# Kernel optimization log

Hardware: AMD Instinct MI355X
Metric: run time of the kernel (lower is better)

Reference implementation:

```python
import jax, jax.numpy as jnp
import numpy as np

DIM = 256
HEADS = 8
HEAD_DIM = DIM // HEADS
B = 4
Wd, Hd = 48, 48
N = Wd * Hd  # 2304


def _layernorm(x, g, b, eps=1e-5):
    mu = jnp.mean(x, axis=-1, keepdims=True)
    var = jnp.mean(jnp.square(x - mu), axis=-1, keepdims=True)
    return (x - mu) * jax.lax.rsqrt(var + eps) * g + b


def _build_mask(mask):
    # Binarize: <1 -> 0, >0 -> 1 (identity on {0,1} inputs)
    m = (mask > 0).astype(jnp.float32)
    flat = m.reshape(B, m.shape[1], Hd * Wd)[:, 0, :]  # [B, N]
    # mask[b,i,j] zeroed where (flat[j]==0 & flat[i]==1) | (flat[j]==0 & flat[i]==0)
    col0 = flat[:, None, :] == 0   # varies along j
    row = flat[:, :, None]         # varies along i
    bad = (col0 & (row == 1)) | (col0 & (row == 0))
    return (~bad).astype(jnp.float32)  # [B, N, N]


def setup_inputs() -> dict:
    key = jax.random.key(0)
    ks = jax.random.split(key, 12)
    s = 0.02
    x = jax.random.normal(ks[0], (B, N, DIM), jnp.float32)
    mask = jax.random.randint(ks[1], (B, 1, Wd, Hd), 0, 2).astype(jnp.float32)
    inp = {
        "x": x,
        "mask": mask,
        "ln_g": jnp.ones((DIM,), jnp.float32),
        "ln_b": jnp.zeros((DIM,), jnp.float32),
        "Wq": jax.random.normal(ks[2], (DIM, DIM), jnp.float32) * s,
        "bq": jnp.zeros((DIM,), jnp.float32),
        "Wk": jax.random.normal(ks[3], (DIM, DIM), jnp.float32) * s,
        "bk": jnp.zeros((DIM,), jnp.float32),
        "Wv": jax.random.normal(ks[4], (DIM, DIM), jnp.float32) * s,
        "bv": jnp.zeros((DIM,), jnp.float32),
        "Wp": jax.random.normal(ks[5], (DIM, DIM), jnp.float32) * s,
        "bp": jnp.zeros((DIM,), jnp.float32),
    }
    return inp


def reference(x, mask, ln_g, ln_b, Wq, bq, Wk, bk, Wv, bv, Wp, bp):
    Bx, Nx, C = x.shape
    mask_f = _build_mask(mask)  # [B, N, N]
    xn = _layernorm(x, ln_g, ln_b)
    def heads(Wm, bm):
        return (xn @ Wm + bm).reshape(Bx, Nx, HEADS, HEAD_DIM).transpose(0, 2, 1, 3)
    q = heads(Wq, bq)
    k = heads(Wk, bk)
    v = heads(Wv, bv)
    # NOTE: no 1/sqrt(d) scaling in the original; multiplicative 0/1 mask pre-softmax
    attn = jnp.einsum("bhnd,bhmd->bhnm", q, k) * mask_f[:, None, :, :]
    attn = jax.nn.softmax(attn, axis=-1)
    out = jnp.einsum("bhnm,bhmd->bhnd", attn, v)
    out = out.transpose(0, 2, 1, 3).reshape(Bx, Nx, C)
    return out @ Wp + bp
```

## Files before the change

kernel.cpp:

```cpp
#include <hip/hip_runtime.h>
#include <math.h>

typedef __attribute__((ext_vector_type(8))) short short8;
typedef __attribute__((ext_vector_type(4))) float f32x4;

#if __has_builtin(__builtin_amdgcn_exp2f)
#define EXP2F(x) __builtin_amdgcn_exp2f(x)
#else
#define EXP2F(x) exp2f(x)
#endif

constexpr int B   = 4;
constexpr int N   = 2304;
constexpr int DIM = 256;
constexpr int NH  = 8;
constexpr int DH  = 32;
constexpr int M   = B * N;
constexpr int SLOTS = 2336;
constexpr int CST = SLOTS * DH;
constexpr int XPB = SLOTS * DIM;
constexpr float LOG2E = 1.44269504088896f;

__device__ inline unsigned short f2bf(float f) {
    union { float f; unsigned u; } c; c.f = f;
    unsigned u = c.u;
    u += 0x7fffu + ((u >> 16) & 1u);
    return (unsigned short)(u >> 16);
}
__device__ inline float bf2f(unsigned short h) {
    union { unsigned u; float f; } c; c.u = ((unsigned)h) << 16;
    return c.f;
}
__device__ inline unsigned bits(float f) {
    union { float f; unsigned u; } c; c.f = f; return c.u;
}

__device__ inline size_t fo256(int r, int k) {
    return ((size_t)((r >> 4) * 8 + (k >> 5)) << 9)
         + (size_t)(((((k & 31) >> 3) << 4) + (r & 15)) * 8 + (k & 7));
}
__device__ inline size_t foQK(int n, int d) {
    return ((size_t)(n >> 4) << 9)
         + (size_t)((((d >> 3) << 4) + (n & 15)) * 8 + (d & 7));
}
__device__ inline size_t foKI(int slot, int d) {
    int tile = ((slot >> 5) << 1) + (slot & 1);
    int npos = (slot & 31) >> 1;
    return ((size_t)tile << 9)
         + (size_t)((((d >> 3) << 4) + npos) * 8 + (d & 7));
}
__device__ inline size_t foVTC(int d, int key) {
    return ((size_t)((d >> 4) * (SLOTS / 32) + (key >> 5)) << 9)
         + (size_t)(((((key & 31) >> 3) << 4) + (d & 15)) * 8 + (key & 7));
}

__global__ __launch_bounds__(256) void scan_kernel(
    const float* __restrict__ mask, int* __restrict__ ncp,
    int* __restrict__ fwd, float* __restrict__ vm,
    unsigned short* __restrict__ xph)
{
    __shared__ int wcnt[9][4];
    __shared__ unsigned long long wbal[9][4];
    int b = blockIdx.x;
    int t = threadIdx.x;
    int wave = t >> 6, lane = t & 63;
    vm[b * 256 + t] = 0.f;
    #pragma unroll
    for (int c = 0; c < 9; ++c) {
        int j = c * 256 + t;
        bool keep = mask[(size_t)b * N + j] > 0.f;
        unsigned long long bal = __ballot(keep);
        if (lane == 0) { wcnt[c][wave] = __popcll(bal); wbal[c][wave] = bal; }
    }
    __syncthreads();
    int Nc = 0;
    #pragma unroll
    for (int c = 0; c < 9; ++c)
        Nc += wcnt[c][0] + wcnt[c][1] + wcnt[c][2] + wcnt[c][3];
    int Nkp = (Nc + 31) & ~31;
    int mend = Nkp + (N - Nc);
    if (t == 0) { ncp[b * 2] = Nc; ncp[b * 2 + 1] = Nkp; }
    int base = 0;
    #pragma unroll
    for (int c = 0; c < 9; ++c) {
        int wb = base;
        for (int w = 0; w < wave; ++w) wb += wcnt[c][w];
        unsigned long long bal = wbal[c][wave];
        bool keep = (bal >> lane) & 1ull;
        int pos = __popcll(bal & ((1ull << lane) - 1ull));
        int keptBefore = wb + pos;
        int j = c * 256 + t;
        fwd[(size_t)b * N + j] = keep ? keptBefore : Nkp + (j - keptBefore);
        base += wcnt[c][0] + wcnt[c][1] + wcnt[c][2] + wcnt[c][3];
    }
    int c1 = Nkp - Nc;
    unsigned short* xb = xph + (size_t)b * XPB;
    for (int u = t; u < 32 * 64; u += 256) {
        int pi = u >> 6;
        int kk = (u & 63) * 4;
        int slot = (pi < c1) ? (Nc + pi) : (mend + (pi - c1));
        ushort4 z4 = {0, 0, 0, 0};
        *(ushort4*)&xb[fo256(slot, kk)] = z4;
    }
}

__global__ __launch_bounds__(256) void prep2(
    const float* __restrict__ x, const float* __restrict__ g,
    const float* __restrict__ bta, const int* __restrict__ fwd,
    const float* __restrict__ Wq, const float* __restrict__ Wk,
    const float* __restrict__ Wv, const float* __restrict__ Wp,
    unsigned short* __restrict__ Wth, unsigned short* __restrict__ Wtl,
    unsigned short* __restrict__ xh, unsigned short* __restrict__ xph)
{
    __shared__ float tbuf[32][33];
    int bx = blockIdx.x;
    int t = threadIdx.x;
    if (bx < 256) {
        int z = bx >> 6, w = bx & 63;
        const float* W = (z == 0) ? Wq : (z == 1) ? Wk : (z == 2) ? Wv : Wp;
        unsigned short* oh = Wth + (size_t)z * DIM * DIM;
        unsigned short* ol = Wtl + (size_t)z * DIM * DIM;
        int tx = t & 31, ty0 = t >> 5;
        int n0 = (w & 7) * 32, k0 = (w >> 3) * 32;
        for (int ty = ty0; ty < 32; ty += 8)
            tbuf[ty][tx] = W[(size_t)(k0 + ty) * DIM + n0 + tx];
        __syncthreads();
        for (int nn = ty0; nn < 32; nn += 8) {
            float v = tbuf[tx][nn];
            unsigned short hh = f2bf(v);
            size_t o = fo256(n0 + nn, k0 + tx);
            oh[o] = hh;
            ol[o] = f2bf(v - bf2f(hh));
        }
    } else {
        int wave = t >> 6, lane = t & 63;
        int row = (bx - 256) * 4 + wave;
        float4 v = *(const float4*)&x[(size_t)row * DIM + lane * 4];
        float s = v.x + v.y + v.z + v.w;
        #pragma unroll
        for (int o = 32; o > 0; o >>= 1) s += __shfl_xor(s, o, 64);
        float mu = s * (1.0f / DIM);
        float d0 = v.x - mu, d1 = v.y - mu, d2 = v.z - mu, d3 = v.w - mu;
        float s2 = d0 * d0 + d1 * d1 + d2 * d2 + d3 * d3;
        #pragma unroll
        for (int o = 32; o > 0; o >>= 1) s2 += __shfl_xor(s2, o, 64);
        float r = rsqrtf(s2 * (1.0f / DIM) + 1e-5f);
        float4 gg = *(const float4*)&g[lane * 4];
        float4 bb = *(const float4*)&bta[lane * 4];
        ushort4 hi;
        hi.x = f2bf(d0 * r * gg.x + bb.x);
        hi.y = f2bf(d1 * r * gg.y + bb.y);
        hi.z = f2bf(d2 * r * gg.z + bb.z);
        hi.w = f2bf(d3 * r * gg.w + bb.w);
        *(ushort4*)&xh[fo256(row, lane * 4)] = hi;
        int b = row / N;
        int slot = fwd[row];
        *(ushort4*)&xph[(size_t)b * XPB + fo256(slot, lane * 4)] = hi;
    }
}

__global__ __launch_bounds__(256, 8) void gemm_qkv(
    const unsigned short* __restrict__ xh,
    const unsigned short* __restrict__ xph,
    const unsigned short* __restrict__ Wth,
    const float* __restrict__ bq, const float* __restrict__ bk,
    const float* __restrict__ bv, const int* __restrict__ ncp,
    unsigned short* __restrict__ qb, unsigned short* __restrict__ kc,
    unsigned short* __restrict__ vc, float* __restrict__ vm)
{
    constexpr size_t WSZ = (size_t)DIM * DIM;
    int z = blockIdx.z, bx = blockIdx.x;
    int tid = threadIdx.x;
    int wave = tid >> 6, lane = tid & 63;
    int quad = lane >> 4, l16 = lane & 15;
    const unsigned short *PA, *PB;
    int arow0, brow0, b;
    if (z == 0) {
        if (bx >= 576) return;
        arow0 = (bx >> 3) * 128 + wave * 32;
        brow0 = (bx & 7) * 32;
        b = ((bx >> 3) * 128) / N;
        PA = xh; PB = Wth;
    } else if (z == 1) {
        b = bx / 152;
        int rr = bx % 152;
        arow0 = (rr >> 3) * 128 + wave * 32;
        brow0 = (rr & 7) * 32;
        if (arow0 >= SLOTS) return;
        if (arow0 >= ncp[b * 2 + 1]) return;
        PA = xph + (size_t)b * XPB;
        PB = Wth + WSZ;
    } else {
        if (bx >= 584) return;
        int nidx = bx % 292;
        b = nidx / 73;
        arow0 = (bx / 292) * 128 + wave * 32;
        brow0 = (nidx % 73) * 32;
        PA = Wth + 2 * WSZ;
        PB = xph + (size_t)b * XPB;
    }
    f32x4 acc[2][2] = {};
    #pragma unroll
    for (int k0 = 0; k0 < DIM; k0 += 32) {
        size_t at = (((size_t)(arow0 >> 4) * 8 + (k0 >> 5)) << 9) + lane * 8;
        size_t bt = (((size_t)(brow0 >> 4) * 8 + (k0 >> 5)) << 9) + lane * 8;
        short8 a0 = *(const short8*)&PA[at];
        short8 a1 = *(const short8*)&PA[at + 4096];
        short8 b0 = *(const short8*)&PB[bt];
        short8 b1 = *(const short8*)&PB[bt + 4096];
        acc[0][0] = __builtin_amdgcn_mfma_f32_16x16x32_bf16(a0, b0, acc[0][0], 0, 0, 0);
        acc[0][1] = __builtin_amdgcn_mfma_f32_16x16x32_bf16(a0, b1, acc[0][1], 0, 0, 0);
        acc[1][0] = __builtin_amdgcn_mfma_f32_16x16x32_bf16(a1, b0, acc[1][0], 0, 0, 0);
        acc[1][1] = __builtin_amdgcn_mfma_f32_16x16x32_bf16(a1, b1, acc[1][1], 0, 0, 0);
    }
    if (z == 0) {
        int nbase = arow0 - b * N;
        #pragma unroll
        for (int j = 0; j < 2; ++j) {
            int c = brow0 + j * 16 + l16;
            int h = c >> 5, d = c & 31;
            float bs = bq[c];
            unsigned short* ob = qb + (size_t)(b * NH + h) * ((size_t)N * DH);
            #pragma unroll
            for (int i = 0; i < 2; ++i)
            #pragma unroll
            for (int r = 0; r < 4; ++r) {
                int n = nbase + i * 16 + quad * 4 + r;
                ob[foQK(n, d)] = f2bf((acc[i][j][r] + bs) * LOG2E);
            }
        }
    } else if (z == 1) {
        #pragma unroll
        for (int j = 0; j < 2; ++j) {
            int c = brow0 + j * 16 + l16;
            int h = c >> 5, d = c & 31;
            float bs = bk[c];
            unsigned short* ob = kc + (size_t)(b * NH + h) * CST;
            #pragma unroll
            for (int i = 0; i < 2; ++i)
            #pragma unroll
            for (int r = 0; r < 4; ++r) {
                int slot = arow0 + i * 16 + quad * 4 + r;
                ob[foKI(slot, d)] = f2bf(acc[i][j][r] + bs);
            }
        }
    } else {
        int Nc  = ncp[b * 2];
        int Nkp = ncp[b * 2 + 1];
        int mend = Nkp + (N - Nc);
        bool anymask = (brow0 + 32 > Nkp) && (brow0 < mend);
        #pragma unroll
        for (int i = 0; i < 2; ++i)
        #pragma unroll
        for (int r = 0; r < 4; ++r) {
            int m = arow0 + i * 16 + quad * 4 + r;
            int h = m >> 5, d = m & 31;
            float bs = bv[m];
            unsigned short* ob = vc + (size_t)(b * NH + h) * CST;
            float vsum = 0.f;
            #pragma unroll
            for (int j = 0; j < 2; ++j) {
                int key = brow0 + j * 16 + l16;
                float val = acc[i][j][r] + bs;
                if (key < Nkp) ob[foVTC(d, key)] = f2bf(val);
                else if (key < mend) vsum += val;
            }
            if (anymask) {
                vsum += __shfl_xor(vsum, 1, 64);
                vsum += __shfl_xor(vsum, 2, 64);
                vsum += __shfl_xor(vsum, 4, 64);
                vsum += __shfl_xor(vsum, 8, 64);
                if (l16 == 0) atomicAdd(&vm[(size_t)(b * NH + h) * 32 + d], vsum);
            }
        }
    }
}

__global__ __launch_bounds__(128, 4) void attn_kernel(
    const unsigned short* __restrict__ Qb,
    const unsigned short* __restrict__ Kc,
    const unsigned short* __restrict__ Vc,
    const int* __restrict__ ncp,
    const float* __restrict__ vm,
    unsigned short* __restrict__ ah)
{
    __shared__ unsigned short pbuf[2 * 2 * 640];
    __shared__ float cbuf[64 * 24];
    int tid  = threadIdx.x;
    int kh   = tid >> 6, lane = tid & 63;
    int quad = lane >> 4, l16 = lane & 15;
    int bh = blockIdx.y, b = bh >> 3, h = bh & 7;

    int q0 = blockIdx.x * 32;
    const unsigned short* Qf = Qb + (size_t)bh * ((size_t)N * DH);
    const unsigned short* Kf = Kc + (size_t)bh * CST;
    const unsigned short* Vf = Vc + (size_t)bh * CST;

    int Nc  = ncp[b * 2];
    int Nkp = ncp[b * 2 + 1];
    int chunks = Nkp >> 5;
    int kbeg = ((chunks * kh) >> 1) << 5;
    int kend = ((chunks * (kh + 1)) >> 1) << 5;

    short8 qA0 = *(const short8*)&Qf[((size_t)(q0 >> 4) << 9) + lane * 8];
    short8 qA1 = *(const short8*)&Qf[((size_t)((q0 >> 4) + 1) << 9) + lane * 8];

    f32x4 o00 = {0,0,0,0}, o01 = {0,0,0,0}, o10 = {0,0,0,0}, o11 = {0,0,0,0};
    float l0[4] = {0,0,0,0}, l1[4] = {0,0,0,0};

    unsigned short* pb0 = &pbuf[(kh * 2 + 0) * 640];
    unsigned short* pb1 = &pbuf[(kh * 2 + 1) * 640];

    short8 kB0 = *(const short8*)&Kf[((size_t)(kbeg >> 4) << 9) + lane * 8];
    short8 kB1 = *(const short8*)&Kf[((size_t)((kbeg >> 4) + 1) << 9) + lane * 8];
    short8 vB0 = *(const short8*)&Vf[((size_t)(kbeg >> 5) << 9) + lane * 8];
    short8 vB1 = *(const short8*)&Vf[((size_t)((SLOTS / 32) + (kbeg >> 5)) << 9) + lane * 8];

    for (int k0 = kbeg; k0 < kend; k0 += 32) {
        int kn = (k0 + 32 < kend) ? k0 + 32 : kbeg;
        short8 nk0 = *(const short8*)&Kf[((size_t)(kn >> 4) << 9) + lane * 8];
        short8 nk1 = *(const short8*)&Kf[((size_t)((kn >> 4) + 1) << 9) + lane * 8];
        short8 nv0 = *(const short8*)&Vf[((size_t)(kn >> 5) << 9) + lane * 8];
        short8 nv1 = *(const short8*)&Vf[((size_t)((SLOTS / 32) + (kn >> 5)) << 9) + lane * 8];

        int key0 = k0 + 2 * l16;
        bool in0 = key0 < Nc;
        bool in1 = key0 + 1 < Nc;
        f32x4 z = {0,0,0,0};
        f32x4 s00 = __builtin_amdgcn_mfma_f32_16x16x32_bf16(qA0, kB0, z, 0, 0, 0);
        f32x4 s01 = __builtin_amdgcn_mfma_f32_16x16x32_bf16(qA0, kB1, z, 0, 0, 0);
        f32x4 s10 = __builtin_amdgcn_mfma_f32_16x16x32_bf16(qA1, kB0, z, 0, 0, 0);
        f32x4 s11 = __builtin_amdgcn_mfma_f32_16x16x32_bf16(qA1, kB1, z, 0, 0, 0);
        #pragma unroll
        for (int r = 0; r < 4; ++r) {
            int row = quad * 4 + r;
            float p00 = in0 ? EXP2F(s00[r]) : 0.f;
            float p01 = in1 ? EXP2F(s01[r]) : 0.f;
            float p10 = in0 ? EXP2F(s10[r]) : 0.f;
            float p11 = in1 ? EXP2F(s11[r]) : 0.f;
            l0[r] += p00 + p01;
            l1[r] += p10 + p11;
            unsigned pk0 = (bits(p00) >> 16) | (bits(p01) & 0xffff0000u);
            unsigned pk1 = (bits(p10) >> 16) | (bits(p11) & 0xffff0000u);
            *(unsigned*)&pb0[row * 40 + 2 * l16] = pk0;
            *(unsigned*)&pb1[row * 40 + 2 * l16] = pk1;
        }
        short8 pA0 = *(const short8*)&pb0[l16 * 40 + quad * 8];
        short8 pA1 = *(const short8*)&pb1[l16 * 40 + quad * 8];
        o00 = __builtin_amdgcn_mfma_f32_16x16x32_bf16(pA0, vB0, o00, 0, 0, 0);
        o01 = __builtin_amdgcn_mfma_f32_16x16x32_bf16(pA0, vB1, o01, 0, 0, 0);
        o10 = __builtin_amdgcn_mfma_f32_16x16x32_bf16(pA1, vB0, o10, 0, 0, 0);
        o11 = __builtin_amdgcn_mfma_f32_16x16x32_bf16(pA1, vB1, o11, 0, 0, 0);

        kB0 = nk0; kB1 = nk1; vB0 = nv0; vB1 = nv1;
    }
    #pragma unroll
    for (int r = 0; r < 4; ++r) {
        #pragma unroll
        for (int off = 1; off < 16; off <<= 1) {
            l0[r] += __shfl_xor(l0[r], off, 64);
            l1[r] += __shfl_xor(l1[r], off, 64);
        }
    }
    if (kh == 1) {
        float* cb = &cbuf[lane * 24];
        *(f32x4*)&cb[0]  = o00;
        *(f32x4*)&cb[4]  = o01;
        *(f32x4*)&cb[8]  = o10;
        *(f32x4*)&cb[12] = o11;
        #pragma unroll
        for (int r = 0; r < 4; ++r) { cb[16 + r] = l0[r]; cb[20 + r] = l1[r]; }
    }
    __syncthreads();
    if (kh == 1) return;
    {
        float* cb = &cbuf[lane * 24];
        o00 += *(f32x4*)&cb[0];
        o01 += *(f32x4*)&cb[4];
        o10 += *(f32x4*)&cb[8];
        o11 += *(f32x4*)&cb[12];
        #pragma unroll
        for (int r = 0; r < 4; ++r) { l0[r] += cb[16 + r]; l1[r] += cb[20 + r]; }
    }
    float vm0 = vm[bh * 32 + l16];
    float vm1 = vm[bh * 32 + 16 + l16];
    float lext = (float)(N - Nc);
    #pragma unroll
    for (int r = 0; r < 4; ++r) {
        int row = quad * 4 + r;
        float ia = 1.f / (l0[r] + lext);
        float ib = 1.f / (l1[r] + lext);
        int ra = b * N + q0 + row;
        int rb = ra + 16;
        ah[fo256(ra, h * 32 + l16)]      = f2bf((o00[r] + vm0) * ia);
        ah[fo256(ra, h * 32 + 16 + l16)] = f2bf((o01[r] + vm1) * ia);
        ah[fo256(rb, h * 32 + l16)]      = f2bf((o10[r] + vm0) * ib);
        ah[fo256(rb, h * 32 + 16 + l16)] = f2bf((o11[r] + vm1) * ib);
    }
}

__global__ __launch_bounds__(256, 8) void gemm_p(
    const unsigned short* __restrict__ Ahi,
    const unsigned short* __restrict__ Wth, const unsigned short* __restrict__ Wtl,
    const float* __restrict__ bias, float* __restrict__ out)
{
    constexpr size_t WSZ = (size_t)DIM * DIM;
    const unsigned short* Bhi = Wth + 3 * WSZ;
    const unsigned short* Blo = Wtl + 3 * WSZ;
    int tid = threadIdx.x;
    int wave = tid >> 6, lane = tid & 63;
    int quad = lane >> 4, l16 = lane & 15;
    int r0 = blockIdx.y * 128 + wave * 32;
    int c0 = blockIdx.x * 16;
    f32x4 acc0 = {}, acc1 = {};
    #pragma unroll
    for (int k0 = 0; k0 < DIM; k0 += 32) {
        size_t at = (((size_t)(r0 >> 4) * 8 + (k0 >> 5)) << 9) + lane * 8;
        size_t bt = (((size_t)(c0 >> 4) * 8 + (k0 >> 5)) << 9) + lane * 8;
        short8 ah0 = *(const short8*)&Ahi[at];
        short8 ah1 = *(const short8*)&Ahi[at + 4096];
        short8 bh = *(const short8*)&Bhi[bt];
        short8 bl = *(const short8*)&Blo[bt];
        acc0 = __builtin_amdgcn_mfma_f32_16x16x32_bf16(ah0, bh, acc0, 0, 0, 0);
        acc0 = __builtin_amdgcn_mfma_f32_16x16x32_bf16(ah0, bl, acc0, 0, 0, 0);
        acc1 = __builtin_amdgcn_mfma_f32_16x16x32_bf16(ah1, bh, acc1, 0, 0, 0);
        acc1 = __builtin_amdgcn_mfma_f32_16x16x32_bf16(ah1, bl, acc1, 0, 0, 0);
    }
    int c = c0 + l16;
    float bs = bias[c];
    #pragma unroll
    for (int r = 0; r < 4; ++r) {
        int R0 = r0 + quad * 4 + r;
        out[(size_t)R0 * DIM + c] = acc0[r] + bs;
        out[(size_t)(R0 + 16) * DIM + c] = acc1[r] + bs;
    }
}

extern "C" void kernel_launch(void* const* d_in, const int* in_sizes, int n_in,
                              void* d_out, int out_size, void* d_ws, size_t ws_size,
                              hipStream_t stream)
{
    const float* x    = (const float*)d_in[0];
    const float* mask = (const float*)d_in[1];
    const float* ln_g = (const float*)d_in[2];
    const float* ln_b = (const float*)d_in[3];
    const float* Wq   = (const float*)d_in[4];
    const float* bq   = (const float*)d_in[5];
    const float* Wk   = (const float*)d_in[6];
    const float* bk   = (const float*)d_in[7];
    const float* Wv   = (const float*)d_in[8];
    const float* bv   = (const float*)d_in[9];
    const float* Wp   = (const float*)d_in[10];
    const float* bp   = (const float*)d_in[11];
    float* out = (float*)d_out;

    constexpr size_t SZ  = (size_t)M * DIM;
    constexpr size_t CSZ = (size_t)B * NH * CST;
    constexpr size_t XSZ = (size_t)B * XPB;
    constexpr size_t WSZ = (size_t)DIM * DIM;
    unsigned short* p = (unsigned short*)d_ws;
    unsigned short* xh = p;  p += SZ;
    unsigned short* xph = p; p += XSZ;
    unsigned short* qb = p;  p += SZ;
    unsigned short* kc = p;  p += CSZ;
    unsigned short* vc = p;  p += CSZ;
    unsigned short* ah = p;  p += SZ;
    unsigned short* wth = p; p += 4 * WSZ;
    unsigned short* wtl = p; p += 4 * WSZ;
    float* vm = (float*)p;
    int* ncp = (int*)(vm + (size_t)B * NH * 32);
    int* fwd = ncp + 2 * B;

    scan_kernel<<<B, 256, 0, stream>>>(mask, ncp, fwd, vm, xph);

    prep2<<<2560, 256, 0, stream>>>(
        x, ln_g, ln_b, fwd, Wq, Wk, Wv, Wp, wth, wtl, xh, xph);

    gemm_qkv<<<dim3(608, 1, 3), 256, 0, stream>>>(
        xh, xph, wth, bq, bk, bv, ncp, qb, kc, vc, vm);

    attn_kernel<<<dim3(N / 32, B * NH), 128, 0, stream>>>(
        qb, kc, vc, ncp, vm, ah);

    gemm_p<<<dim3(DIM / 16, M / 128), 256, 0, stream>>>(
        ah, wth, wtl, bp, out);
}
```

Before: 148.1 us.

## Merge mask scan into prep kernel and scatter K/V compaction in GEMM epilogue

The separate mask-scan kernel is removed and its work becomes four extra blocks of a single prep kernel. The permuted copy of the normalized activations (xph) is dropped; the QKV GEMM now reads the original rows and scatters K and V outputs to compacted slots through the forward index map in its epilogue. The masked-key V sum is accumulated for every tile instead of only boundary tiles. The attention kernel's manual bf16 truncation is replaced with a hardware packed convert. This saves one launch and a large activation copy, but the K GEMM now computes all rows instead of skipping padded ones, and the scatter stores are less contiguous.

Measured after the change: 146.3 us. No clear change (-1.2%).

```diff
diff --git a/kernel.cpp b/kernel.cpp
--- a/kernel.cpp
+++ b/kernel.cpp
@@ -18,7 +18,6 @@
 constexpr int M   = B * N;
 constexpr int SLOTS = 2336;
 constexpr int CST = SLOTS * DH;
-constexpr int XPB = SLOTS * DIM;
 constexpr float LOG2E = 1.44269504088896f;
 
 __device__ inline unsigned short f2bf(float f) {
@@ -31,9 +30,6 @@
     union { unsigned u; float f; } c; c.u = ((unsigned)h) << 16;
     return c.f;
 }
-__device__ inline unsigned bits(float f) {
-    union { float f; unsigned u; } c; c.f = f; return c.u;
-}
 
 __device__ inline size_t fo256(int r, int k) {
     return ((size_t)((r >> 4) * 8 + (k >> 5)) << 9)
@@ -54,69 +50,45 @@
          + (size_t)(((((key & 31) >> 3) << 4) + (d & 15)) * 8 + (key & 7));
 }
 
-__global__ __launch_bounds__(256) void scan_kernel(
-    const float* __restrict__ mask, int* __restrict__ ncp,
-    int* __restrict__ fwd, float* __restrict__ vm,
-    unsigned short* __restrict__ xph)
-{
-    __shared__ int wcnt[9][4];
-    __shared__ unsigned long long wbal[9][4];
-    int b = blockIdx.x;
-    int t = threadIdx.x;
-    int wave = t >> 6, lane = t & 63;
-    vm[b * 256 + t] = 0.f;
-    #pragma unroll
-    for (int c = 0; c < 9; ++c) {
-        int j = c * 256 + t;
-        bool keep = mask[(size_t)b * N + j] > 0.f;
-        unsigned long long bal = __ballot(keep);
-        if (lane == 0) { wcnt[c][wave] = __popcll(bal); wbal[c][wave] = bal; }
-    }
-    __syncthreads();
-    int Nc = 0;
-    #pragma unroll
-    for (int c = 0; c < 9; ++c)
-        Nc += wcnt[c][0] + wcnt[c][1] + wcnt[c][2] + wcnt[c][3];
-    int Nkp = (Nc + 31) & ~31;
-    int mend = Nkp + (N - Nc);
-    if (t == 0) { ncp[b * 2] = Nc; ncp[b * 2 + 1] = Nkp; }
-    int base = 0;
-    #pragma unroll
-    for (int c = 0; c < 9; ++c) {
-        int wb = base;
-        for (int w = 0; w < wave; ++w) wb += wcnt[c][w];
-        unsigned long long bal = wbal[c][wave];
-        bool keep = (bal >> lane) & 1ull;
-        int pos = __popcll(bal & ((1ull << lane) - 1ull));
-        int keptBefore = wb + pos;
-        int j = c * 256 + t;
-        fwd[(size_t)b * N + j] = keep ? keptBefore : Nkp + (j - keptBefore);
-        base += wcnt[c][0] + wcnt[c][1] + wcnt[c][2] + wcnt[c][3];
-    }
-    int c1 = Nkp - Nc;
-    unsigned short* xb = xph + (size_t)b * XPB;
-    for (int u = t; u < 32 * 64; u += 256) {
-        int pi = u >> 6;
-        int kk = (u & 63) * 4;
-        int slot = (pi < c1) ? (Nc + pi) : (mend + (pi - c1));
-        ushort4 z4 = {0, 0, 0, 0};
-        *(ushort4*)&xb[fo256(slot, kk)] = z4;
-    }
-}
-
-__global__ __launch_bounds__(256) void prep2(
+__global__ __launch_bounds__(256) void prep_kernel(
     const float* __restrict__ x, const float* __restrict__ g,
-    const float* __restrict__ bta, const int* __restrict__ fwd,
+    const float* __restrict__ bta, unsigned short* __restrict__ xh,
     const float* __restrict__ Wq, const float* __restrict__ Wk,
     const float* __restrict__ Wv, const float* __restrict__ Wp,
     unsigned short* __restrict__ Wth, unsigned short* __restrict__ Wtl,
-    unsigned short* __restrict__ xh, unsigned short* __restrict__ xph)
+    const float* __restrict__ mask, int* __restrict__ ncp,
+    int* __restrict__ fwd, float* __restrict__ vm,
+    unsigned short* __restrict__ vc)
 {
     __shared__ float tbuf[32][33];
+    __shared__ int wcnt[9][4];
+    __shared__ unsigned long long wbal[9][4];
     int bx = blockIdx.x;
     int t = threadIdx.x;
-    if (bx < 256) {
-        int z = bx >> 6, w = bx & 63;
+    int wave = t >> 6, lane = t & 63;
+    if (bx < 2304) {
+        int row = bx * 4 + wave;
+        float4 v = *(const float4*)&x[(size_t)row * DIM + lane * 4];
+        float s = v.x + v.y + v.z + v.w;
+        #pragma unroll
+        for (int o = 32; o > 0; o >>= 1) s += __shfl_xor(s, o, 64);
+        float mu = s * (1.0f / DIM);
+        float d0 = v.x - mu, d1 = v.y - mu, d2 = v.z - mu, d3 = v.w - mu;
+        float s2 = d0 * d0 + d1 * d1 + d2 * d2 + d3 * d3;
+        #pragma unroll
+        for (int o = 32; o > 0; o >>= 1) s2 += __shfl_xor(s2, o, 64);
+        float r = rsqrtf(s2 * (1.0f / DIM) + 1e-5f);
+        float4 gg = *(const float4*)&g[lane * 4];
+        float4 bb = *(const float4*)&bta[lane * 4];
+        ushort4 hi;
+        hi.x = f2bf(d0 * r * gg.x + bb.x);
+        hi.y = f2bf(d1 * r * gg.y + bb.y);
+        hi.z = f2bf(d2 * r * gg.z + bb.z);
+        hi.w = f2bf(d3 * r * gg.w + bb.w);
+        *(ushort4*)&xh[fo256(row, lane * 4)] = hi;
+    } else if (bx < 2560) {
+        int idx = bx - 2304;
+        int z = idx >> 6, w = idx & 63;
         const float* W = (z == 0) ? Wq : (z == 1) ? Wk : (z == 2) ? Wv : Wp;
         unsigned short* oh = Wth + (size_t)z * DIM * DIM;
         unsigned short* ol = Wtl + (size_t)z * DIM * DIM;
@@ -133,38 +105,51 @@
             ol[o] = f2bf(v - bf2f(hh));
         }
     } else {
-        int wave = t >> 6, lane = t & 63;
-        int row = (bx - 256) * 4 + wave;
-        float4 v = *(const float4*)&x[(size_t)row * DIM + lane * 4];
-        float s = v.x + v.y + v.z + v.w;
-        #pragma unroll
-        for (int o = 32; o > 0; o >>= 1) s += __shfl_xor(s, o, 64);
-        float mu = s * (1.0f / DIM);
-        float d0 = v.x - mu, d1 = v.y - mu, d2 = v.z - mu, d3 = v.w - mu;
-        float s2 = d0 * d0 + d1 * d1 + d2 * d2 + d3 * d3;
-        #pragma unroll
-        for (int o = 32; o > 0; o >>= 1) s2 += __shfl_xor(s2, o, 64);
-        float r = rsqrtf(s2 * (1.0f / DIM) + 1e-5f);
-        float4 gg = *(const float4*)&g[lane * 4];
-        float4 bb = *(const float4*)&bta[lane * 4];
-        ushort4 hi;
-        hi.x = f2bf(d0 * r * gg.x + bb.x);
-        hi.y = f2bf(d1 * r * gg.y + bb.y);
-        hi.z = f2bf(d2 * r * gg.z + bb.z);
-        hi.w = f2bf(d3 * r * gg.w + bb.w);
-        *(ushort4*)&xh[fo256(row, lane * 4)] = hi;
-        int b = row / N;
-        int slot = fwd[row];
-        *(ushort4*)&xph[(size_t)b * XPB + fo256(slot, lane * 4)] = hi;
+        int b = bx - 2560;
+        vm[b * 256 + t] = 0.f;
+        #pragma unroll
+        for (int c = 0; c < 9; ++c) {
+            int j = c * 256 + t;
+            bool keep = mask[(size_t)b * N + j] > 0.f;
+            unsigned long long bal = __ballot(keep);
+            if (lane == 0) { wcnt[c][wave] = __popcll(bal); wbal[c][wave] = bal; }
+        }
+        __syncthreads();
+        int Nc = 0;
+        #pragma unroll
+        for (int c = 0; c < 9; ++c)
+            Nc += wcnt[c][0] + wcnt[c][1] + wcnt[c][2] + wcnt[c][3];
+        int Nkp = (Nc + 31) & ~31;
+        if (t == 0) { ncp[b * 2] = Nc; ncp[b * 2 + 1] = Nkp; }
+        int base = 0;
+        #pragma unroll
+        for (int c = 0; c < 9; ++c) {
+            int wb = base;
+            for (int w = 0; w < wave; ++w) wb += wcnt[c][w];
+            unsigned long long bal = wbal[c][wave];
+            bool keep = (bal >> lane) & 1ull;
+            int pos = __popcll(bal & ((1ull << lane) - 1ull));
+            int keptBefore = wb + pos;
+            int j = c * 256 + t;
+            fwd[(size_t)b * N + j] = keep ? keptBefore : Nkp + (j - keptBefore);
+            base += wcnt[c][0] + wcnt[c][1] + wcnt[c][2] + wcnt[c][3];
+        }
+        int npad = Nkp - Nc;
+        for (int u = t; u < npad * 256; u += 256) {
+            int pi = u >> 8;
+            int hd = u & 255;
+            int h = hd >> 5, d = hd & 31;
+            vc[(size_t)(b * NH + h) * CST + foVTC(d, Nc + pi)] = 0;
+        }
     }
 }
 
 __global__ __launch_bounds__(256, 8) void gemm_qkv(
     const unsigned short* __restrict__ xh,
-    const unsigned short* __restrict__ xph,
     const unsigned short* __restrict__ Wth,
     const float* __restrict__ bq, const float* __restrict__ bk,
     const float* __restrict__ bv, const int* __restrict__ ncp,
+    const int* __restrict__ fwd,
     unsigned short* __restrict__ qb, unsigned short* __restrict__ kc,
     unsigned short* __restrict__ vc, float* __restrict__ vm)
 {
@@ -175,29 +160,19 @@
     int quad = lane >> 4, l16 = lane & 15;
     const unsigned short *PA, *PB;
     int arow0, brow0, b;
-    if (z == 0) {
-        if (bx >= 576) return;
+    if (z == 2) {
+        int nidx = bx % 288;
+        b = nidx / 72;
+        arow0 = (bx / 288) * 128 + wave * 32;
+        brow0 = b * N + (nidx % 72) * 32;
+        PA = Wth + 2 * WSZ;
+        PB = xh;
+    } else {
         arow0 = (bx >> 3) * 128 + wave * 32;
         brow0 = (bx & 7) * 32;
-        b = ((bx >> 3) * 128) / N;
-        PA = xh; PB = Wth;
-    } else if (z == 1) {
-        b = bx / 152;
-        int rr = bx % 152;
-        arow0 = (rr >> 3) * 128 + wave * 32;
-        brow0 = (rr & 7) * 32;
-        if (arow0 >= SLOTS) return;
-        if (arow0 >= ncp[b * 2 + 1]) return;
-        PA = xph + (size_t)b * XPB;
-        PB = Wth + WSZ;
-    } else {
-        if (bx >= 584) return;
-        int nidx = bx % 292;
-        b = nidx / 73;
-        arow0 = (bx / 292) * 128 + wave * 32;
-        brow0 = (nidx % 73) * 32;
-        PA = Wth + 2 * WSZ;
-        PB = xph + (size_t)b * XPB;
+        b = arow0 / N;
+        PA = xh;
+        PB = Wth + (size_t)z * WSZ;
     }
     f32x4 acc[2][2] = {};
     #pragma unroll
@@ -230,25 +205,27 @@
             }
         }
     } else if (z == 1) {
-        #pragma unroll
-        for (int j = 0; j < 2; ++j) {
-            int c = brow0 + j * 16 + l16;
-            int h = c >> 5, d = c & 31;
-            float bs = bk[c];
-            unsigned short* ob = kc + (size_t)(b * NH + h) * CST;
+        int Nkp = ncp[b * 2 + 1];
+        #pragma unroll
+        for (int i = 0; i < 2; ++i) {
+            int4 f4 = *(const int4*)&fwd[arow0 + i * 16 + quad * 4];
             #pragma unroll
-            for (int i = 0; i < 2; ++i)
-            #pragma unroll
-            for (int r = 0; r < 4; ++r) {
-                int slot = arow0 + i * 16 + quad * 4 + r;
-                ob[foKI(slot, d)] = f2bf(acc[i][j][r] + bs);
+            for (int j = 0; j < 2; ++j) {
+                int c = brow0 + j * 16 + l16;
+                int h = c >> 5, d = c & 31;
+                float bs = bk[c];
+                unsigned short* ob = kc + (size_t)(b * NH + h) * CST;
+                #pragma unroll
+                for (int r = 0; r < 4; ++r) {
+                    int slot = (&f4.x)[r];
+                    if (slot < Nkp) ob[foKI(slot, d)] = f2bf(acc[i][j][r] + bs);
+                }
             }
         }
     } else {
-        int Nc  = ncp[b * 2];
         int Nkp = ncp[b * 2 + 1];
-        int mend = Nkp + (N - Nc);
-        bool anymask = (brow0 + 32 > Nkp) && (brow0 < mend);
+        int s0 = fwd[brow0 + l16];
+        int s1 = fwd[brow0 + 16 + l16];
         #pragma unroll
         for (int i = 0; i < 2; ++i)
         #pragma unroll
@@ -260,18 +237,17 @@
             float vsum = 0.f;
             #pragma unroll
             for (int j = 0; j < 2; ++j) {
-                int key = brow0 + j * 16 + l16;
+                int slot = j ? s1 : s0;
                 float val = acc[i][j][r] + bs;
-                if (key < Nkp) ob[foVTC(d, key)] = f2bf(val);
-                else if (key < mend) vsum += val;
+                if (slot < Nkp) ob[foVTC(d, slot)] = f2bf(val);
+                else vsum += val;
             }
-            if (anymask) {
-                vsum += __shfl_xor(vsum, 1, 64);
-                vsum += __shfl_xor(vsum, 2, 64);
-                vsum += __shfl_xor(vsum, 4, 64);
-                vsum += __shfl_xor(vsum, 8, 64);
-                if (l16 == 0) atomicAdd(&vm[(size_t)(b * NH + h) * 32 + d], vsum);
-            }
+            vsum += __shfl_xor(vsum, 1, 64);
+            vsum += __shfl_xor(vsum, 2, 64);
+            vsum += __shfl_xor(vsum, 4, 64);
+            vsum += __shfl_xor(vsum, 8, 64);
+            if (l16 == 0 && vsum != 0.f)
+                atomicAdd(&vm[(size_t)(b * NH + h) * 32 + d], vsum);
         }
     }
 }
@@ -340,8 +316,9 @@
             float p11 = in1 ? EXP2F(s11[r]) : 0.f;
             l0[r] += p00 + p01;
             l1[r] += p10 + p11;
-            unsigned pk0 = (bits(p00) >> 16) | (bits(p01) & 0xffff0000u);
-            unsigned pk1 = (bits(p10) >> 16) | (bits(p11) & 0xffff0000u);
+            unsigned pk0, pk1;
+            asm("v_cvt_pk_bf16_f32 %0, %1, %2" : "=v"(pk0) : "v"(p00), "v"(p01));
+            asm("v_cvt_pk_bf16_f32 %0, %1, %2" : "=v"(pk1) : "v"(p10), "v"(p11));
             *(unsigned*)&pb0[row * 40 + 2 * l16] = pk0;
             *(unsigned*)&pb1[row * 40 + 2 * l16] = pk1;
         }
@@ -456,11 +433,9 @@
 
     constexpr size_t SZ  = (size_t)M * DIM;
     constexpr size_t CSZ = (size_t)B * NH * CST;
-    constexpr size_t XSZ = (size_t)B * XPB;
     constexpr size_t WSZ = (size_t)DIM * DIM;
     unsigned short* p = (unsigned short*)d_ws;
     unsigned short* xh = p;  p += SZ;
-    unsigned short* xph = p; p += XSZ;
     unsigned short* qb = p;  p += SZ;
     unsigned short* kc = p;  p += CSZ;
     unsigned short* vc = p;  p += CSZ;
@@ -471,13 +446,11 @@
     int* ncp = (int*)(vm + (size_t)B * NH * 32);
     int* fwd = ncp + 2 * B;
 
-    scan_kernel<<<B, 256, 0, stream>>>(mask, ncp, fwd, vm, xph);
-
-    prep2<<<2560, 256, 0, stream>>>(
-        x, ln_g, ln_b, fwd, Wq, Wk, Wv, Wp, wth, wtl, xh, xph);
-
-    gemm_qkv<<<dim3(608, 1, 3), 256, 0, stream>>>(
-        xh, xph, wth, bq, bk, bv, ncp, qb, kc, vc, vm);
+    prep_kernel<<<2564, 256, 0, stream>>>(
+        x, ln_g, ln_b, xh, Wq, Wk, Wv, Wp, wth, wtl, mask, ncp, fwd, vm, vc);
+
+    gemm_qkv<<<dim3(576, 1, 3), 256, 0, stream>>>(
+        xh, wth, bq, bk, bv, ncp, fwd, qb, kc, vc, vm);
 
     attn_kernel<<<dim3(N / 32, B * NH), 128, 0, stream>>>(
         qb, kc, vc, ncp, vm, ah);
```
